# Performance work log

Hardware: AMD Instinct MI355X
Metric: run time of the kernel (lower is better)

## Reference

```python
import jax, jax.numpy as jnp
import numpy as np

EPS = 1e-6
TOP_K = 2


def setup_inputs() -> dict:
    key = jax.random.key(0)
    k0, k1, k2, k3, k4 = jax.random.split(key, 5)
    B, S, H, I, E = 1, 2048, 1024, 3584, 8
    return {
        "hidden_states": jax.random.normal(k0, (B, S, H), jnp.float32),
        "rms_weight": jnp.ones((H,), jnp.float32),
        "gate_w": jax.random.normal(k1, (E, H), jnp.float32) * (H ** -0.5),
        "w1": jax.random.normal(k2, (E, I, H), jnp.float32) * (H ** -0.5),
        "w2": jax.random.normal(k3, (E, H, I), jnp.float32) * (I ** -0.5),
        "w3": jax.random.normal(k4, (E, I, H), jnp.float32) * (H ** -0.5),
    }


def reference(hidden_states, rms_weight, gate_w, w1, w2, w3):
    B, S, H = hidden_states.shape
    E = gate_w.shape[0]
    # RMSNorm (fp32 internally, matches _RMSNorm)
    x = hidden_states.astype(jnp.float32)
    var = jnp.mean(x * x, axis=-1, keepdims=True)
    h = rms_weight * (x * jax.lax.rsqrt(var + EPS))  # [B,S,H]
    # Router: softmax over experts, top-k, renormalize
    logits = jnp.einsum('bsh,eh->bse', h, gate_w)
    scores = jax.nn.softmax(logits.astype(jnp.float32), axis=-1)
    top_w, top_i = jax.lax.top_k(scores, TOP_K)        # [B,S,K]
    top_w = top_w / jnp.sum(top_w, axis=-1, keepdims=True)
    top_w = top_w.astype(h.dtype)
    # Per-token combine weight for every expert: cw[t,e]
    hf = h.reshape(-1, H)                               # [T,H]
    oh = jax.nn.one_hot(top_i.reshape(-1, TOP_K), E, dtype=h.dtype)  # [T,K,E]
    cw = jnp.einsum('tke,tk->te', oh, top_w.reshape(-1, TOP_K))       # [T,E]
    # SwiGLU expert MLPs, batched over experts (dense dispatch; weights zero out unrouted tokens)
    a = jnp.einsum('th,eih->eti', hf, w1)               # [E,T,I]
    g = jnp.einsum('th,eih->eti', hf, w3)               # [E,T,I]
    eo = jnp.einsum('eti,ehi->eth', jax.nn.silu(a) * g, w2)  # [E,T,H]
    out = jnp.einsum('eth,te->th', eo, cw)              # [T,H]
    return hidden_states + out.reshape(B, S, H)
```

## Files before the change

### kernel.cpp

```cpp
#include <hip/hip_runtime.h>
#include <hip/hip_bf16.h>
#include <stdint.h>

#define T_TOK 2048
#define HDIM  1024
#define IDIM  3584
#define NEXP  8
#define NROWS 4096

typedef __attribute__((ext_vector_type(8))) short bf16x8;
typedef __attribute__((ext_vector_type(4))) float f32x4;

typedef __attribute__((address_space(3))) unsigned lds_u32;
typedef const __attribute__((address_space(1))) unsigned glb_u32;

#define MFMA16 __builtin_amdgcn_mfma_f32_16x16x32_bf16

__device__ __forceinline__ unsigned short f2bf(float f){
  union { float f; unsigned u; } v; v.f = f;
  unsigned r = v.u + 0x7FFFu + ((v.u >> 16) & 1u);
  return (unsigned short)(r >> 16);
}
__device__ __forceinline__ bf16x8 pack8(float4 lo, float4 hi){
  union { __hip_bfloat162 b2[4]; bf16x8 v; } u;
  u.b2[0] = __float22bfloat162_rn(float2{lo.x, lo.y});
  u.b2[1] = __float22bfloat162_rn(float2{lo.z, lo.w});
  u.b2[2] = __float22bfloat162_rn(float2{hi.x, hi.y});
  u.b2[3] = __float22bfloat162_rn(float2{hi.z, hi.w});
  return u.v;
}

__global__ __launch_bounds__(256) void k_rms_router(
    const float* __restrict__ x, const float* __restrict__ rmsw,
    const float* __restrict__ gw, unsigned short* __restrict__ h_bf,
    int* __restrict__ topk_i, float* __restrict__ topk_w, int* __restrict__ count)
{
  const int t = blockIdx.x, tid = threadIdx.x;
  const int lane = tid & 63, wid = tid >> 6;
  float4 x4 = reinterpret_cast<const float4*>(x)[t*256 + tid];
  float ss = x4.x*x4.x + x4.y*x4.y + x4.z*x4.z + x4.w*x4.w;
  #pragma unroll
  for (int o = 32; o >= 1; o >>= 1) ss += __shfl_xor(ss, o);
  __shared__ float sred[4];
  __shared__ float slog[32];
  if (lane == 0) sred[wid] = ss;
  __syncthreads();
  float inv = rsqrtf((sred[0]+sred[1]+sred[2]+sred[3]) * (1.0f/HDIM) + 1e-6f);
  float4 w4 = reinterpret_cast<const float4*>(rmsw)[tid];
  float h0 = x4.x*inv*w4.x, h1 = x4.y*inv*w4.y, h2 = x4.z*inv*w4.z, h3 = x4.w*inv*w4.w;
  ushort4 hb; hb.x = f2bf(h0); hb.y = f2bf(h1); hb.z = f2bf(h2); hb.w = f2bf(h3);
  reinterpret_cast<ushort4*>(h_bf)[t*256 + tid] = hb;
  #pragma unroll
  for (int e = 0; e < NEXP; e++){
    float4 g4 = reinterpret_cast<const float4*>(gw)[e*256 + tid];
    float v = h0*g4.x + h1*g4.y + h2*g4.z + h3*g4.w;
    #pragma unroll
    for (int o = 32; o >= 1; o >>= 1) v += __shfl_xor(v, o);
    if (lane == 0) slog[e*4 + wid] = v;
  }
  __syncthreads();
  if (tid == 0){
    float lg[NEXP];
    #pragma unroll
    for (int e = 0; e < NEXP; e++) lg[e] = slog[e*4]+slog[e*4+1]+slog[e*4+2]+slog[e*4+3];
    int i0 = 0;
    for (int e = 1; e < NEXP; e++) if (lg[e] > lg[i0]) i0 = e;
    int i1 = -1;
    for (int e = 0; e < NEXP; e++){ if (e == i0) continue; if (i1 < 0 || lg[e] > lg[i1]) i1 = e; }
    float m  = fmaxf(lg[i0], lg[i1]);
    float e0 = expf(lg[i0]-m), e1 = expf(lg[i1]-m);
    float s  = e0 + e1;
    topk_i[t*2] = i0; topk_i[t*2+1] = i1;
    topk_w[t*2] = e0/s; topk_w[t*2+1] = e1/s;
    atomicAdd(&count[i0], 1); atomicAdd(&count[i1], 1);
  }
}

__global__ void k_scan(const int* __restrict__ count, int* __restrict__ offset){
  if (threadIdx.x == 0){
    int o = 0;
    for (int e = 0; e < NEXP; e++){ offset[e] = o; o += count[e]; }
  }
}

__global__ __launch_bounds__(256) void k_scatter(
    const int* __restrict__ topk_i, const float* __restrict__ topk_w,
    const int* __restrict__ offset, int* __restrict__ cursor,
    int* __restrict__ token_of_row, float* __restrict__ wrow, int* __restrict__ slot_of)
{
  int t = blockIdx.x*256 + threadIdx.x;
  if (t >= T_TOK) return;
  #pragma unroll
  for (int k = 0; k < 2; k++){
    int e = topk_i[t*2+k];
    int pos = atomicAdd(&cursor[e], 1);
    int row = offset[e] + pos;
    token_of_row[row] = t;
    wrow[row] = topk_w[t*2+k];
    slot_of[t*2+k] = row;
  }
}

__global__ __launch_bounds__(256, 3) void k_mlp_in(
    const unsigned short* __restrict__ h_bf, const float* __restrict__ w1,
    const float* __restrict__ w3, const int* __restrict__ token_of_row,
    const int* __restrict__ count, const int* __restrict__ offset,
    unsigned short* __restrict__ act)
{
  const int d = blockIdx.x;
  const int e = d & 7;
  const int q = d >> 3;
  const int panel = q >> 4;
  const int rt = q & 15;
  const int cnt = count[e];
  if (rt * 128 >= cnt) return;
  const int off = offset[e], row0 = off + rt*128, rend = off + cnt;
  const int col0 = panel * 64;
  const int tid = threadIdx.x, lane = tid & 63, wid = tid >> 6;
  const int wave_r = wid >> 1, wave_c = wid & 1;

  __shared__ __align__(16) char sA [16384];
  __shared__ __align__(16) char sB1[16384];
  __shared__ __align__(16) char sB3[16384];

  const int srow = tid >> 3;
  const int sg   = (tid & 7) ^ (srow & 7);
  const unsigned short* aptr[4];
  #pragma unroll
  for (int j = 0; j < 4; j++){
    int tok = token_of_row[min(row0 + srow + 32*j, NROWS-1)];
    aptr[j] = h_bf + (size_t)tok*HDIM + sg*8;
  }
  const int bl = (tid & 15) ^ ((tid >> 4) & 15);
  const float* b1base = w1 + ((size_t)e*IDIM + col0 + (tid >> 4))*HDIM + bl*4;
  const float* b3base = w3 + ((size_t)e*IDIM + col0 + (tid >> 4))*HDIM + bl*4;

  #define ISSUE(kk) {                                                                \
    _Pragma("unroll")                                                                \
    for (int j = 0; j < 4; j++)                                                      \
      __builtin_amdgcn_global_load_lds((glb_u32*)(const void*)(aptr[j] + (kk)*64),   \
          (lds_u32*)(void*)(sA + j*4096 + tid*16), 16, 0, 0);                        \
    _Pragma("unroll")                                                                \
    for (int j = 0; j < 4; j++){                                                     \
      __builtin_amdgcn_global_load_lds(                                              \
          (glb_u32*)(const void*)(b1base + (size_t)j*16*HDIM + (kk)*64),             \
          (lds_u32*)(void*)(sB1 + j*4096 + tid*16), 16, 0, 0);                       \
      __builtin_amdgcn_global_load_lds(                                              \
          (glb_u32*)(const void*)(b3base + (size_t)j*16*HDIM + (kk)*64),             \
          (lds_u32*)(void*)(sB3 + j*4096 + tid*16), 16, 0, 0);                       \
    } }

  f32x4 acc1[4][2], acc3[4][2];
  #pragma unroll
  for (int m = 0; m < 4; m++)
    #pragma unroll
    for (int n = 0; n < 2; n++){
      acc1[m][n] = (f32x4){0.f,0.f,0.f,0.f};
      acc3[m][n] = (f32x4){0.f,0.f,0.f,0.f};
    }

  for (int kk = 0; kk < HDIM/64; kk++){
    ISSUE(kk);
    __syncthreads();
    #pragma unroll
    for (int ki = 0; ki < 2; ki++){
      bf16x8 af[4];
      #pragma unroll
      for (int m = 0; m < 4; m++){
        int row = wave_r*64 + m*16 + (lane & 15);
        int slot = ki*4 + (lane >> 4);
        af[m] = *reinterpret_cast<const bf16x8*>(sA + row*128 + ((slot ^ (row&7))<<4));
      }
      #pragma unroll
      for (int n = 0; n < 2; n++){
        int c  = wave_c*32 + n*16 + (lane & 15);
        int l0 = ki*8 + (lane >> 4)*2;
        int p0 = (l0     ^ (c & 15)) << 4;
        int p1 = ((l0+1) ^ (c & 15)) << 4;
        float4 lo1 = *reinterpret_cast<const float4*>(sB1 + c*256 + p0);
        float4 hi1 = *reinterpret_cast<const float4*>(sB1 + c*256 + p1);
        float4 lo3 = *reinterpret_cast<const float4*>(sB3 + c*256 + p0);
        float4 hi3 = *reinterpret_cast<const float4*>(sB3 + c*256 + p1);
        bf16x8 b1 = pack8(lo1, hi1);
        bf16x8 b3 = pack8(lo3, hi3);
        #pragma unroll
        for (int m = 0; m < 4; m++){
          acc1[m][n] = MFMA16(af[m], b1, acc1[m][n], 0,0,0);
          acc3[m][n] = MFMA16(af[m], b3, acc3[m][n], 0,0,0);
        }
      }
    }
    __syncthreads();
  }

  const int lcol = lane & 15, lrow4 = (lane >> 4) * 4;
  #pragma unroll
  for (int m = 0; m < 4; m++){
    #pragma unroll
    for (int n = 0; n < 2; n++){
      int gcol = col0 + wave_c*32 + n*16 + lcol;
      #pragma unroll
      for (int r = 0; r < 4; r++){
        int grow = row0 + wave_r*64 + m*16 + lrow4 + r;
        if (grow < rend){
          float a = acc1[m][n][r], g = acc3[m][n][r];
          float sig = 1.0f / (1.0f + __expf(-a));
          act[(size_t)grow*IDIM + gcol] = f2bf(a * sig * g);
        }
      }
    }
  }
  #undef ISSUE
}

__global__ __launch_bounds__(256, 4) void k_mlp_out(
    const unsigned short* __restrict__ act, const float* __restrict__ w2,
    const float* __restrict__ wrow, const int* __restrict__ count,
    const int* __restrict__ offset, float* __restrict__ eo)
{
  const int d = blockIdx.x;
  const int e = d & 7;
  const int q = d >> 3;
  const int panel = q >> 4;
  const int rt = q & 15;
  const int cnt = count[e];
  if (rt * 128 >= cnt) return;
  const int off = offset[e], row0 = off + rt*128, rend = off + cnt;
  const int col0 = panel * 64;
  const int tid = threadIdx.x, lane = tid & 63, wid = tid >> 6;
  const int wave_r = wid >> 1, wave_c = wid & 1;

  __shared__ __align__(16) char sA[16384];
  __shared__ __align__(16) char sB[16384];

  const int srow = tid >> 3;
  const int sg   = (tid & 7) ^ (srow & 7);
  const unsigned short* aptr[4];
  #pragma unroll
  for (int j = 0; j < 4; j++){
    int r = min(row0 + srow + 32*j, NROWS-1);
    aptr[j] = act + (size_t)r*IDIM + sg*8;
  }
  const int bl = (tid & 15) ^ ((tid >> 4) & 15);
  const float* bbase = w2 + ((size_t)e*HDIM + col0 + (tid >> 4))*IDIM + bl*4;

  #define ISSUE(kk) {                                                                \
    _Pragma("unroll")                                                                \
    for (int j = 0; j < 4; j++)                                                      \
      __builtin_amdgcn_global_load_lds((glb_u32*)(const void*)(aptr[j] + (kk)*64),   \
          (lds_u32*)(void*)(sA + j*4096 + tid*16), 16, 0, 0);                        \
    _Pragma("unroll")                                                                \
    for (int j = 0; j < 4; j++)                                                      \
      __builtin_amdgcn_global_load_lds(                                              \
          (glb_u32*)(const void*)(bbase + (size_t)j*16*IDIM + (kk)*64),              \
          (lds_u32*)(void*)(sB + j*4096 + tid*16), 16, 0, 0); }

  f32x4 acc[4][2];
  #pragma unroll
  for (int m = 0; m < 4; m++)
    #pragma unroll
    for (int n = 0; n < 2; n++) acc[m][n] = (f32x4){0.f,0.f,0.f,0.f};

  for (int kk = 0; kk < IDIM/64; kk++){
    ISSUE(kk);
    __syncthreads();
    #pragma unroll
    for (int ki = 0; ki < 2; ki++){
      bf16x8 af[4];
      #pragma unroll
      for (int m = 0; m < 4; m++){
        int row = wave_r*64 + m*16 + (lane & 15);
        int slot = ki*4 + (lane >> 4);
        af[m] = *reinterpret_cast<const bf16x8*>(sA + row*128 + ((slot ^ (row&7))<<4));
      }
      #pragma unroll
      for (int n = 0; n < 2; n++){
        int c  = wave_c*32 + n*16 + (lane & 15);
        int l0 = ki*8 + (lane >> 4)*2;
        int p0 = (l0     ^ (c & 15)) << 4;
        int p1 = ((l0+1) ^ (c & 15)) << 4;
        float4 lo = *reinterpret_cast<const float4*>(sB + c*256 + p0);
        float4 hi = *reinterpret_cast<const float4*>(sB + c*256 + p1);
        bf16x8 fb = pack8(lo, hi);
        #pragma unroll
        for (int m = 0; m < 4; m++)
          acc[m][n] = MFMA16(af[m], fb, acc[m][n], 0,0,0);
      }
    }
    __syncthreads();
  }

  const int lcol = lane & 15, lrow4 = (lane >> 4) * 4;
  #pragma unroll
  for (int m = 0; m < 4; m++){
    #pragma unroll
    for (int n = 0; n < 2; n++){
      int gcol = col0 + wave_c*32 + n*16 + lcol;
      #pragma unroll
      for (int r = 0; r < 4; r++){
        int grow = row0 + wave_r*64 + m*16 + lrow4 + r;
        if (grow < rend){
          eo[(size_t)grow*HDIM + gcol] = acc[m][n][r] * wrow[grow];
        }
      }
    }
  }
  #undef ISSUE
}

__global__ __launch_bounds__(256) void k_combine(
    const float* __restrict__ x, const float* __restrict__ eo,
    const int* __restrict__ slot_of, float* __restrict__ out)
{
  const int t = blockIdx.x, tid = threadIdx.x;
  const int s0 = slot_of[t*2], s1 = slot_of[t*2+1];
  float4 xv = reinterpret_cast<const float4*>(x)[t*256 + tid];
  float4 a  = reinterpret_cast<const float4*>(eo)[s0*256 + tid];
  float4 b  = reinterpret_cast<const float4*>(eo)[s1*256 + tid];
  float4 ov;
  ov.x = xv.x + a.x + b.x;
  ov.y = xv.y + a.y + b.y;
  ov.z = xv.z + a.z + b.z;
  ov.w = xv.w + a.w + b.w;
  reinterpret_cast<float4*>(out)[t*256 + tid] = ov;
}

extern "C" void kernel_launch(void* const* d_in, const int* in_sizes, int n_in,
                              void* d_out, int out_size, void* d_ws, size_t ws_size,
                              hipStream_t stream)
{
  const float* x    = (const float*)d_in[0];
  const float* rmsw = (const float*)d_in[1];
  const float* gw   = (const float*)d_in[2];
  const float* w1   = (const float*)d_in[3];
  const float* w2   = (const float*)d_in[4];
  const float* w3   = (const float*)d_in[5];
  float* out = (float*)d_out;

  char* ws = (char*)d_ws;
  size_t o = 0;
  auto alloc = [&](size_t bytes) -> void* {
    void* p = ws + o;
    o += (bytes + 255) & ~(size_t)255;
    return p;
  };
  unsigned short* h_bf   = (unsigned short*)alloc((size_t)T_TOK*HDIM*2);
  int*   topk_i          = (int*)  alloc(T_TOK*2*4);
  float* topk_w          = (float*)alloc(T_TOK*2*4);
  int*   counters        = (int*)  alloc(64*4);
  int*   token_of_row    = (int*)  alloc(NROWS*4);
  float* wrow            = (float*)alloc(NROWS*4);
  int*   slot_of         = (int*)  alloc(T_TOK*2*4);
  unsigned short* act    = (unsigned short*)alloc((size_t)NROWS*IDIM*2);
  float* eo              = (float*)alloc((size_t)NROWS*HDIM*4);
  int* count  = counters;
  int* cursor = counters + 8;
  int* offset = counters + 16;

  hipMemsetAsync(counters, 0, 64*4, stream);
  k_rms_router<<<T_TOK, 256, 0, stream>>>(x, rmsw, gw, h_bf, topk_i, topk_w, count);
  k_scan<<<1, 64, 0, stream>>>(count, offset);
  k_scatter<<<(T_TOK+255)/256, 256, 0, stream>>>(topk_i, topk_w, offset, cursor,
                                                 token_of_row, wrow, slot_of);
  k_mlp_in <<<7168, 256, 0, stream>>>(h_bf, w1, w3, token_of_row, count, offset, act);
  k_mlp_out<<<2048, 256, 0, stream>>>(act, w2, wrow, count, offset, eo);
  k_combine<<<T_TOK, 256, 0, stream>>>(x, eo, slot_of, out);
}
```

Baseline: 364.0 us.

## Pre-convert expert weights to bf16 and schedule GEMMs over a compact job list

After: 298.6 us. 18.0% less time.

```diff
diff --git a/kernel.cpp b/kernel.cpp
--- a/kernel.cpp
+++ b/kernel.cpp
@@ -7,6 +7,9 @@
 #define IDIM  3584
 #define NEXP  8
 #define NROWS 4096
+#define WELEM 29360128
+#define NJOBS 40
+#define CVTB  512
 
 typedef __attribute__((ext_vector_type(8))) short bf16x8;
 typedef __attribute__((ext_vector_type(4))) float f32x4;
@@ -21,19 +24,17 @@
   unsigned r = v.u + 0x7FFFu + ((v.u >> 16) & 1u);
   return (unsigned short)(r >> 16);
 }
-__device__ __forceinline__ bf16x8 pack8(float4 lo, float4 hi){
-  union { __hip_bfloat162 b2[4]; bf16x8 v; } u;
-  u.b2[0] = __float22bfloat162_rn(float2{lo.x, lo.y});
-  u.b2[1] = __float22bfloat162_rn(float2{lo.z, lo.w});
-  u.b2[2] = __float22bfloat162_rn(float2{hi.x, hi.y});
-  u.b2[3] = __float22bfloat162_rn(float2{hi.z, hi.w});
-  return u.v;
+__device__ __forceinline__ unsigned cvt2(float a, float b){
+  __hip_bfloat162 h = __float22bfloat162_rn(float2{a, b});
+  return *reinterpret_cast<unsigned*>(&h);
 }
 
 __global__ __launch_bounds__(256) void k_rms_router(
     const float* __restrict__ x, const float* __restrict__ rmsw,
     const float* __restrict__ gw, unsigned short* __restrict__ h_bf,
-    int* __restrict__ topk_i, float* __restrict__ topk_w, int* __restrict__ count)
+    int* __restrict__ topk_i, float* __restrict__ topk_w, int* __restrict__ count,
+    const float4* __restrict__ w1s, const float4* __restrict__ w3s,
+    uint2* __restrict__ w1d, uint2* __restrict__ w3d)
 {
   const int t = blockIdx.x, tid = threadIdx.x;
   const int lane = tid & 63, wid = tid >> 6;
@@ -74,12 +75,26 @@
     topk_w[t*2] = e0/s; topk_w[t*2+1] = e1/s;
     atomicAdd(&count[i0], 1); atomicAdd(&count[i1], 1);
   }
-}
-
-__global__ void k_scan(const int* __restrict__ count, int* __restrict__ offset){
+  const int stride = 2048*256;
+  for (int i = t*256 + tid; i < WELEM/4; i += stride){
+    float4 a = w1s[i];
+    w1d[i] = make_uint2(cvt2(a.x, a.y), cvt2(a.z, a.w));
+    float4 b = w3s[i];
+    w3d[i] = make_uint2(cvt2(b.x, b.y), cvt2(b.z, b.w));
+  }
+}
+
+__global__ void k_scan(const int* __restrict__ count, int* __restrict__ offset,
+                       int* __restrict__ jobs){
   if (threadIdx.x == 0){
-    int o = 0;
-    for (int e = 0; e < NEXP; e++){ offset[e] = o; o += count[e]; }
+    int o = 0, L = 0;
+    for (int e = 0; e < NEXP; e++){
+      offset[e] = o;
+      int nrt = (count[e] + 127) >> 7;
+      for (int r = 0; r < nrt && L < NJOBS; r++) jobs[L++] = (e << 8) | r;
+      o += count[e];
+    }
+    for (; L < NJOBS; L++) jobs[L] = -1;
   }
 }
 
@@ -101,39 +116,67 @@
   }
 }
 
+__global__ __launch_bounds__(256) void k_cvt(
+    const float4* __restrict__ src, uint2* __restrict__ dst, int n4)
+{
+  int stride = gridDim.x * blockDim.x;
+  for (int i = blockIdx.x*blockDim.x + threadIdx.x; i < n4; i += stride){
+    float4 v = src[i];
+    dst[i] = make_uint2(cvt2(v.x, v.y), cvt2(v.z, v.w));
+  }
+}
+
 __global__ __launch_bounds__(256, 3) void k_mlp_in(
-    const unsigned short* __restrict__ h_bf, const float* __restrict__ w1,
-    const float* __restrict__ w3, const int* __restrict__ token_of_row,
+    const unsigned short* __restrict__ h_bf, const unsigned short* __restrict__ w1bf,
+    const unsigned short* __restrict__ w3bf, const int* __restrict__ token_of_row,
     const int* __restrict__ count, const int* __restrict__ offset,
-    unsigned short* __restrict__ act)
+    const int* __restrict__ jobs, unsigned short* __restrict__ act,
+    const float4* __restrict__ w2s, uint2* __restrict__ w2d)
 {
   const int d = blockIdx.x;
-  const int e = d & 7;
-  const int q = d >> 3;
-  const int panel = q >> 4;
-  const int rt = q & 15;
+  const int tid = threadIdx.x;
+  if (d >= NJOBS*56){
+    if (w2d){
+      int i0 = (d - NJOBS*56)*256 + tid;
+      for (int i = i0; i < WELEM/4; i += CVTB*256){
+        float4 v = w2s[i];
+        w2d[i] = make_uint2(cvt2(v.x, v.y), cvt2(v.z, v.w));
+      }
+    }
+    return;
+  }
+  const int p = d % 56;
+  const int t = d / 56;
+  const int job = jobs[t];
+  if (job < 0) return;
+  const int e = job >> 8, rt = job & 255;
   const int cnt = count[e];
-  if (rt * 128 >= cnt) return;
   const int off = offset[e], row0 = off + rt*128, rend = off + cnt;
-  const int col0 = panel * 64;
-  const int tid = threadIdx.x, lane = tid & 63, wid = tid >> 6;
+  const int col0 = p * 64;
+  const int lane = tid & 63, wid = tid >> 6;
   const int wave_r = wid >> 1, wave_c = wid & 1;
 
   __shared__ __align__(16) char sA [16384];
-  __shared__ __align__(16) char sB1[16384];
-  __shared__ __align__(16) char sB3[16384];
+  __shared__ __align__(16) char sB1[8192];
+  __shared__ __align__(16) char sB2[8192];
 
   const int srow = tid >> 3;
   const int sg   = (tid & 7) ^ (srow & 7);
+
   const unsigned short* aptr[4];
   #pragma unroll
   for (int j = 0; j < 4; j++){
     int tok = token_of_row[min(row0 + srow + 32*j, NROWS-1)];
     aptr[j] = h_bf + (size_t)tok*HDIM + sg*8;
   }
-  const int bl = (tid & 15) ^ ((tid >> 4) & 15);
-  const float* b1base = w1 + ((size_t)e*IDIM + col0 + (tid >> 4))*HDIM + bl*4;
-  const float* b3base = w3 + ((size_t)e*IDIM + col0 + (tid >> 4))*HDIM + bl*4;
+  const unsigned short* b1ptr[2];
+  const unsigned short* b3ptr[2];
+  #pragma unroll
+  for (int j = 0; j < 2; j++){
+    int col = col0 + srow + 32*j;
+    b1ptr[j] = w1bf + (size_t)(e*IDIM + col)*HDIM + sg*8;
+    b3ptr[j] = w3bf + (size_t)(e*IDIM + col)*HDIM + sg*8;
+  }
 
   #define ISSUE(kk) {                                                                \
     _Pragma("unroll")                                                                \
@@ -141,13 +184,11 @@
       __builtin_amdgcn_global_load_lds((glb_u32*)(const void*)(aptr[j] + (kk)*64),   \
           (lds_u32*)(void*)(sA + j*4096 + tid*16), 16, 0, 0);                        \
     _Pragma("unroll")                                                                \
-    for (int j = 0; j < 4; j++){                                                     \
-      __builtin_amdgcn_global_load_lds(                                              \
-          (glb_u32*)(const void*)(b1base + (size_t)j*16*HDIM + (kk)*64),             \
+    for (int j = 0; j < 2; j++){                                                     \
+      __builtin_amdgcn_global_load_lds((glb_u32*)(const void*)(b1ptr[j] + (kk)*64),  \
           (lds_u32*)(void*)(sB1 + j*4096 + tid*16), 16, 0, 0);                       \
-      __builtin_amdgcn_global_load_lds(                                              \
-          (glb_u32*)(const void*)(b3base + (size_t)j*16*HDIM + (kk)*64),             \
-          (lds_u32*)(void*)(sB3 + j*4096 + tid*16), 16, 0, 0);                       \
+      __builtin_amdgcn_global_load_lds((glb_u32*)(const void*)(b3ptr[j] + (kk)*64),  \
+          (lds_u32*)(void*)(sB2 + j*4096 + tid*16), 16, 0, 0);                       \
     } }
 
   f32x4 acc1[4][2], acc3[4][2];
@@ -173,20 +214,14 @@
       }
       #pragma unroll
       for (int n = 0; n < 2; n++){
-        int c  = wave_c*32 + n*16 + (lane & 15);
-        int l0 = ki*8 + (lane >> 4)*2;
-        int p0 = (l0     ^ (c & 15)) << 4;
-        int p1 = ((l0+1) ^ (c & 15)) << 4;
-        float4 lo1 = *reinterpret_cast<const float4*>(sB1 + c*256 + p0);
-        float4 hi1 = *reinterpret_cast<const float4*>(sB1 + c*256 + p1);
-        float4 lo3 = *reinterpret_cast<const float4*>(sB3 + c*256 + p0);
-        float4 hi3 = *reinterpret_cast<const float4*>(sB3 + c*256 + p1);
-        bf16x8 b1 = pack8(lo1, hi1);
-        bf16x8 b3 = pack8(lo3, hi3);
+        int col = wave_c*32 + n*16 + (lane & 15);
+        int slot = ki*4 + (lane >> 4);
+        bf16x8 b1 = *reinterpret_cast<const bf16x8*>(sB1 + col*128 + ((slot ^ (col&7))<<4));
+        bf16x8 b2 = *reinterpret_cast<const bf16x8*>(sB2 + col*128 + ((slot ^ (col&7))<<4));
         #pragma unroll
         for (int m = 0; m < 4; m++){
           acc1[m][n] = MFMA16(af[m], b1, acc1[m][n], 0,0,0);
-          acc3[m][n] = MFMA16(af[m], b3, acc3[m][n], 0,0,0);
+          acc3[m][n] = MFMA16(af[m], b2, acc3[m][n], 0,0,0);
         }
       }
     }
@@ -213,46 +248,51 @@
   #undef ISSUE
 }
 
-__global__ __launch_bounds__(256, 4) void k_mlp_out(
-    const unsigned short* __restrict__ act, const float* __restrict__ w2,
+__global__ __launch_bounds__(256, 3) void k_mlp_out(
+    const unsigned short* __restrict__ act, const unsigned short* __restrict__ w2bf,
     const float* __restrict__ wrow, const int* __restrict__ count,
-    const int* __restrict__ offset, float* __restrict__ eo)
+    const int* __restrict__ offset, const int* __restrict__ jobs,
+    float* __restrict__ eo)
 {
   const int d = blockIdx.x;
-  const int e = d & 7;
-  const int q = d >> 3;
-  const int panel = q >> 4;
-  const int rt = q & 15;
+  const int p = d & 15;
+  const int t = d >> 4;
+  const int job = jobs[t];
+  if (job < 0) return;
+  const int e = job >> 8, rt = job & 255;
   const int cnt = count[e];
-  if (rt * 128 >= cnt) return;
   const int off = offset[e], row0 = off + rt*128, rend = off + cnt;
-  const int col0 = panel * 64;
+  const int col0 = p * 64;
   const int tid = threadIdx.x, lane = tid & 63, wid = tid >> 6;
   const int wave_r = wid >> 1, wave_c = wid & 1;
 
-  __shared__ __align__(16) char sA[16384];
+  __shared__ __align__(16) char sA[32768];
   __shared__ __align__(16) char sB[16384];
 
-  const int srow = tid >> 3;
-  const int sg   = (tid & 7) ^ (srow & 7);
-  const unsigned short* aptr[4];
+  const int sr16 = tid >> 4;
+  const int sg   = (tid & 15) ^ sr16;
+
+  const unsigned short* aptr[8];
+  #pragma unroll
+  for (int j = 0; j < 8; j++){
+    int r = min(row0 + j*16 + sr16, NROWS-1);
+    aptr[j] = act + (size_t)r*IDIM + sg*8;
+  }
+  const unsigned short* bptr[4];
   #pragma unroll
   for (int j = 0; j < 4; j++){
-    int r = min(row0 + srow + 32*j, NROWS-1);
-    aptr[j] = act + (size_t)r*IDIM + sg*8;
-  }
-  const int bl = (tid & 15) ^ ((tid >> 4) & 15);
-  const float* bbase = w2 + ((size_t)e*HDIM + col0 + (tid >> 4))*IDIM + bl*4;
+    int col = col0 + j*16 + sr16;
+    bptr[j] = w2bf + (size_t)(e*HDIM + col)*IDIM + sg*8;
+  }
 
   #define ISSUE(kk) {                                                                \
     _Pragma("unroll")                                                                \
-    for (int j = 0; j < 4; j++)                                                      \
-      __builtin_amdgcn_global_load_lds((glb_u32*)(const void*)(aptr[j] + (kk)*64),   \
+    for (int j = 0; j < 8; j++)                                                      \
+      __builtin_amdgcn_global_load_lds((glb_u32*)(const void*)(aptr[j] + (kk)*128),  \
           (lds_u32*)(void*)(sA + j*4096 + tid*16), 16, 0, 0);                        \
     _Pragma("unroll")                                                                \
     for (int j = 0; j < 4; j++)                                                      \
-      __builtin_amdgcn_global_load_lds(                                              \
-          (glb_u32*)(const void*)(bbase + (size_t)j*16*IDIM + (kk)*64),              \
+      __builtin_amdgcn_global_load_lds((glb_u32*)(const void*)(bptr[j] + (kk)*128),  \
           (lds_u32*)(void*)(sB + j*4096 + tid*16), 16, 0, 0); }
 
   f32x4 acc[4][2];
@@ -261,27 +301,23 @@
     #pragma unroll
     for (int n = 0; n < 2; n++) acc[m][n] = (f32x4){0.f,0.f,0.f,0.f};
 
-  for (int kk = 0; kk < IDIM/64; kk++){
+  for (int kk = 0; kk < IDIM/128; kk++){
     ISSUE(kk);
     __syncthreads();
     #pragma unroll
-    for (int ki = 0; ki < 2; ki++){
+    for (int ki = 0; ki < 4; ki++){
       bf16x8 af[4];
       #pragma unroll
       for (int m = 0; m < 4; m++){
         int row = wave_r*64 + m*16 + (lane & 15);
         int slot = ki*4 + (lane >> 4);
-        af[m] = *reinterpret_cast<const bf16x8*>(sA + row*128 + ((slot ^ (row&7))<<4));
+        af[m] = *reinterpret_cast<const bf16x8*>(sA + row*256 + ((slot ^ (row&15))<<4));
       }
       #pragma unroll
       for (int n = 0; n < 2; n++){
-        int c  = wave_c*32 + n*16 + (lane & 15);
-        int l0 = ki*8 + (lane >> 4)*2;
-        int p0 = (l0     ^ (c & 15)) << 4;
-        int p1 = ((l0+1) ^ (c & 15)) << 4;
-        float4 lo = *reinterpret_cast<const float4*>(sB + c*256 + p0);
-        float4 hi = *reinterpret_cast<const float4*>(sB + c*256 + p1);
-        bf16x8 fb = pack8(lo, hi);
+        int col = wave_c*32 + n*16 + (lane & 15);
+        int slot = ki*4 + (lane >> 4);
+        bf16x8 fb = *reinterpret_cast<const bf16x8*>(sB + col*256 + ((slot ^ (col&15))<<4));
         #pragma unroll
         for (int m = 0; m < 4; m++)
           acc[m][n] = MFMA16(af[m], fb, acc[m][n], 0,0,0);
@@ -348,6 +384,7 @@
   int*   topk_i          = (int*)  alloc(T_TOK*2*4);
   float* topk_w          = (float*)alloc(T_TOK*2*4);
   int*   counters        = (int*)  alloc(64*4);
+  int*   jobs            = (int*)  alloc(NJOBS*4);
   int*   token_of_row    = (int*)  alloc(NROWS*4);
   float* wrow            = (float*)alloc(NROWS*4);
   int*   slot_of         = (int*)  alloc(T_TOK*2*4);
@@ -357,12 +394,23 @@
   int* cursor = counters + 8;
   int* offset = counters + 16;
 
+  bool have3 = (ws_size >= o + (size_t)3*WELEM*2);
+  unsigned short* w1bf = (unsigned short*)(ws + o);
+  unsigned short* w3bf = w1bf + WELEM;
+  unsigned short* w2bf = have3 ? (w3bf + WELEM) : w1bf;
+
   hipMemsetAsync(counters, 0, 64*4, stream);
-  k_rms_router<<<T_TOK, 256, 0, stream>>>(x, rmsw, gw, h_bf, topk_i, topk_w, count);
-  k_scan<<<1, 64, 0, stream>>>(count, offset);
+  k_rms_router<<<T_TOK, 256, 0, stream>>>(x, rmsw, gw, h_bf, topk_i, topk_w, count,
+                                          (const float4*)w1, (const float4*)w3,
+                                          (uint2*)w1bf, (uint2*)w3bf);
+  k_scan<<<1, 64, 0, stream>>>(count, offset, jobs);
   k_scatter<<<(T_TOK+255)/256, 256, 0, stream>>>(topk_i, topk_w, offset, cursor,
                                                  token_of_row, wrow, slot_of);
-  k_mlp_in <<<7168, 256, 0, stream>>>(h_bf, w1, w3, token_of_row, count, offset, act);
-  k_mlp_out<<<2048, 256, 0, stream>>>(act, w2, wrow, count, offset, eo);
+  k_mlp_in<<<NJOBS*56 + (have3 ? CVTB : 0), 256, 0, stream>>>(
+      h_bf, w1bf, w3bf, token_of_row, count, offset, jobs, act,
+      (const float4*)w2, have3 ? (uint2*)w2bf : (uint2*)nullptr);
+  if (!have3)
+    k_cvt<<<2048, 256, 0, stream>>>((const float4*)w2, (uint2*)w2bf, WELEM/4);
+  k_mlp_out<<<NJOBS*16, 256, 0, stream>>>(act, w2bf, wrow, count, offset, jobs, eo);
   k_combine<<<T_TOK, 256, 0, stream>>>(x, eo, slot_of, out);
 }
```
